# Kernel optimization log

Measured on AMD Instinct MI355X. Metric: run time of the kernel, lower is better.

## Reference

```python
import jax, jax.numpy as jnp
import numpy as np

N_EMBD = 768
N_HEAD = 12
HEAD_DIM = N_EMBD // N_HEAD
EPS = 1e-5


def _ln(x, g, b):
    mu = jnp.mean(x, axis=-1, keepdims=True)
    var = jnp.mean(jnp.square(x - mu), axis=-1, keepdims=True)
    return (x - mu) * jax.lax.rsqrt(var + EPS) * g + b


def _gelu(x):
    # GPT-2 / BERT tanh-approximate GELU (new_gelu)
    c = jnp.sqrt(2.0 / jnp.pi).astype(x.dtype)
    return 0.5 * x * (1.0 + jnp.tanh(c * (x + 0.044715 * x * x * x)))


def setup_inputs() -> dict:
    key = jax.random.key(0)
    ks = jax.random.split(key, 8)
    B, T, C = 4, 2048, N_EMBD
    s = 0.02
    return {
        "x": jax.random.normal(ks[0], (B, T, C), jnp.float32),
        "attention_mask": jnp.ones((B, T), jnp.float32),
        "ln1_g": jnp.ones((C,), jnp.float32),
        "ln1_b": jnp.zeros((C,), jnp.float32),
        "ln2_g": jnp.ones((C,), jnp.float32),
        "ln2_b": jnp.zeros((C,), jnp.float32),
        "W_attn": jax.random.normal(ks[1], (C, 3 * C), jnp.float32) * s,
        "b_attn": jnp.zeros((3 * C,), jnp.float32),
        "W_proj": jax.random.normal(ks[2], (C, C), jnp.float32) * s,
        "b_proj": jnp.zeros((C,), jnp.float32),
        "W_fc": jax.random.normal(ks[3], (C, 4 * C), jnp.float32) * s,
        "b_fc": jnp.zeros((4 * C,), jnp.float32),
        "W_out": jax.random.normal(ks[4], (4 * C, C), jnp.float32) * s,
        "b_out": jnp.zeros((C,), jnp.float32),
    }


def reference(x, attention_mask, ln1_g, ln1_b, ln2_g, ln2_b,
              W_attn, b_attn, W_proj, b_proj, W_fc, b_fc, W_out, b_out):
    B, T, C = x.shape
    H, D = N_HEAD, HEAD_DIM

    # --- attention sublayer ---
    h = _ln(x, ln1_g, ln1_b)
    qkv = h @ W_attn + b_attn                      # [B,T,3C]
    q, k, v = jnp.split(qkv, 3, axis=-1)
    q = q.reshape(B, T, H, D).transpose(0, 2, 1, 3)  # [B,H,T,D]
    k = k.reshape(B, T, H, D).transpose(0, 2, 1, 3)
    v = v.reshape(B, T, H, D).transpose(0, 2, 1, 3)

    att = jnp.einsum('bhqd,bhkd->bhqk', q, k) * (1.0 / jnp.sqrt(D).astype(x.dtype))
    mask_add = (1.0 - attention_mask)[:, None, None, :] * -10000.0  # [B,1,1,T]
    att = att + mask_add
    att = jax.nn.softmax(att, axis=-1)
    y = jnp.einsum('bhqk,bhkd->bhqd', att, v)      # [B,H,T,D]
    y = y.transpose(0, 2, 1, 3).reshape(B, T, C)
    x = x + (y @ W_proj + b_proj)

    # --- MLP sublayer ---
    h = _ln(x, ln2_g, ln2_b)
    h = _gelu(h @ W_fc + b_fc)
    x = x + (h @ W_out + b_out)
    return x
```

## Files before the change

### kernel.cpp

```cpp
#include <hip/hip_runtime.h>
#include <hip/hip_bf16.h>
#include <cstdint>

using short8   = __attribute__((ext_vector_type(8))) short;
using floatx4  = __attribute__((ext_vector_type(4))) float;
using ushort4v = __attribute__((ext_vector_type(4))) unsigned short;

#define DEVI static __device__ __forceinline__

DEVI unsigned short f2bf(float f) {
    union { float f; unsigned u; } v; v.f = f;
    unsigned r = v.u + 0x7FFFu + ((v.u >> 16) & 1u);
    return (unsigned short)(r >> 16);
}

DEVI unsigned cvtpk_bf16(float lo, float hi) {
    unsigned r;
    asm("v_cvt_pk_bf16_f32 %0, %1, %2" : "=v"(r) : "v"(lo), "v"(hi));
    return r;
}

typedef const __attribute__((address_space(1))) unsigned int gas_uint;
typedef __attribute__((address_space(3))) unsigned int las_uint;

DEVI void gload16(const void* g, void* l) {
    __builtin_amdgcn_global_load_lds((gas_uint*)g, (las_uint*)l, 16, 0, 0);
}

DEVI float gelu_f(float x) {
    float z = 0.7978845608028654f * (x + 0.044715f * x * x * x);
    float e = __expf(2.0f * z);
    float t = 1.0f - 2.0f / (e + 1.0f);
    return 0.5f * x * (1.0f + t);
}

#define QSCALE 0.18033688011112042f

__global__ __launch_bounds__(256)
void transpose_cast(const float* __restrict__ W, unsigned short* __restrict__ Wt,
                    int K, int N)
{
    __shared__ float tile[32][33];
    const int n0 = blockIdx.x * 32, k0 = blockIdx.y * 32;
    const int tx = threadIdx.x & 31, ty = threadIdx.x >> 5;
#pragma unroll
    for (int j = 0; j < 4; ++j)
        tile[ty + j * 8][tx] = W[(long)(k0 + ty + j * 8) * N + n0 + tx];
    __syncthreads();
#pragma unroll
    for (int j = 0; j < 4; ++j)
        Wt[(long)(n0 + ty + j * 8) * K + k0 + tx] = f2bf(tile[tx][ty + j * 8]);
}

__global__ __launch_bounds__(256)
void ln_cast_k(const float* __restrict__ x, const float* __restrict__ g,
               const float* __restrict__ beta, unsigned short* __restrict__ out)
{
    const int row = blockIdx.x;
    const int tid = threadIdx.x;
    const float* xr = x + (long)row * 768;
    float v0 = xr[tid], v1 = xr[tid + 256], v2 = xr[tid + 512];
    float s  = v0 + v1 + v2;
    float sq = v0 * v0 + v1 * v1 + v2 * v2;
#pragma unroll
    for (int m = 1; m < 64; m <<= 1) {
        s  += __shfl_xor(s, m);
        sq += __shfl_xor(sq, m);
    }
    __shared__ float ss[4], ssq[4];
    if ((tid & 63) == 0) { ss[tid >> 6] = s; ssq[tid >> 6] = sq; }
    __syncthreads();
    s  = ss[0] + ss[1] + ss[2] + ss[3];
    sq = ssq[0] + ssq[1] + ssq[2] + ssq[3];
    const float mean = s * (1.0f / 768.0f);
    const float var  = sq * (1.0f / 768.0f) - mean * mean;
    const float rstd = rsqrtf(var + 1e-5f);
    unsigned short* orow = out + (long)row * 768;
    orow[tid]       = f2bf((v0 - mean) * rstd * g[tid]       + beta[tid]);
    orow[tid + 256] = f2bf((v1 - mean) * rstd * g[tid + 256] + beta[tid + 256]);
    orow[tid + 512] = f2bf((v2 - mean) * rstd * g[tid + 512] + beta[tid + 512]);
}

template<int EPI>
__global__ __launch_bounds__(256)
void gemm128(const unsigned short* __restrict__ A,
             const unsigned short* __restrict__ Bt,
             const float* __restrict__ bias,
             const float* __restrict__ resid,
             unsigned short* __restrict__ ob0,
             unsigned short* __restrict__ ob1,
             unsigned short* __restrict__ ob2,
             float* __restrict__ of,
             int K, int N)
{
    const int mt = blockIdx.x, nt = blockIdx.y;
    const int tid = threadIdx.x;
    const int w = tid >> 6, lane = tid & 63;
    const int l16 = lane & 15, lq = lane >> 4;
    const int wm = w >> 1, wn = w & 1;

    __shared__ unsigned short As[128 * 64];
    __shared__ unsigned short Bs[128 * 64];

    const floatx4 fzero = {0.f, 0.f, 0.f, 0.f};
    floatx4 acc[4][4];
#pragma unroll
    for (int i = 0; i < 4; ++i)
#pragma unroll
        for (int j = 0; j < 4; ++j) acc[i][j] = fzero;

    const char* Abyte = (const char*)A + (long)mt * 128 * K * 2;
    const char* Bbyte = (const char*)Bt + (long)nt * 128 * K * 2;
    const int KT = K >> 6;

    for (int kt = 0; kt < KT; ++kt) {
        const int kbyte = kt * 128;
#pragma unroll
        for (int r4 = 0; r4 < 4; ++r4) {
            int base = (w * 4 + r4) * 1024;
            int loff = base + lane * 16;
            int row  = loff >> 7;
            int scb  = (loff & 127) ^ ((row & 7) << 4);
            gload16(Abyte + (long)row * (K * 2) + kbyte + scb, (char*)As + base);
            gload16(Bbyte + (long)row * (K * 2) + kbyte + scb, (char*)Bs + base);
        }
        __syncthreads();
#pragma unroll
        for (int ks = 0; ks < 2; ++ks) {
            const int kb = ks * 64 + lq * 16;
            short8 af[4], bfr[4];
#pragma unroll
            for (int f = 0; f < 4; ++f) {
                int ar = wm * 64 + f * 16 + l16;
                af[f]  = *(const short8*)((const char*)As + ar * 128 + (kb ^ ((ar & 7) << 4)));
                int br = wn * 64 + f * 16 + l16;
                bfr[f] = *(const short8*)((const char*)Bs + br * 128 + (kb ^ ((br & 7) << 4)));
            }
#pragma unroll
            for (int i = 0; i < 4; ++i)
#pragma unroll
                for (int j = 0; j < 4; ++j)
                    acc[i][j] = __builtin_amdgcn_mfma_f32_16x16x32_bf16(af[i], bfr[j], acc[i][j], 0, 0, 0);
        }
        __syncthreads();
    }

    const int col0 = nt * 128 + wn * 64;
    const int row0 = mt * 128 + wm * 64;
#pragma unroll
    for (int j = 0; j < 4; ++j) {
        const int col = col0 + j * 16 + l16;
        const float bv = bias[col];
#pragma unroll
        for (int i = 0; i < 4; ++i) {
            const int rowb = row0 + i * 16 + lq * 4;
            float v[4];
#pragma unroll
            for (int r = 0; r < 4; ++r) v[r] = acc[i][j][r] + bv;

            if (EPI == 0) {
                const int which = (col >= 1536) ? 2 : (col >= 768 ? 1 : 0);
                const int c = col - which * 768;
                const int hh = c >> 6, d = c & 63;
                const int bb = rowb >> 11;
                const int t  = rowb & 2047;
                if (which == 2) {
                    ushort4v pk;
#pragma unroll
                    for (int r = 0; r < 4; ++r) pk[r] = f2bf(v[r]);
                    const int tlo = t & 31;
                    const int tS  = (t & ~31) + ((tlo & 12) << 1) + ((tlo & 16) >> 2);
                    long vi = ((long)(bb * 12 + hh) * 64 + d) * 2048 + tS;
                    *(ushort4v*)(ob2 + vi) = pk;
                } else {
                    unsigned short* dst = (which == 0) ? ob0 : ob1;
                    const float qs = (which == 0) ? QSCALE : 1.0f;
                    long base = ((long)(bb * 12 + hh) * 2048 + t) * 64 + d;
#pragma unroll
                    for (int r = 0; r < 4; ++r) dst[base + (long)r * 64] = f2bf(v[r] * qs);
                }
            } else if (EPI == 1 || EPI == 3) {
#pragma unroll
                for (int r = 0; r < 4; ++r) {
                    long idx = (long)(rowb + r) * N + col;
                    of[idx] = v[r] + resid[idx];
                }
            } else {
#pragma unroll
                for (int r = 0; r < 4; ++r) {
                    long idx = (long)(rowb + r) * N + col;
                    ob0[idx] = f2bf(gelu_f(v[r]));
                }
            }
        }
    }
}

__global__ __launch_bounds__(256)
void attn_fwd(const unsigned short* __restrict__ q,
              const unsigned short* __restrict__ k,
              const unsigned short* __restrict__ vt,
              const float* __restrict__ mask,
              unsigned short* __restrict__ y)
{
    const int qt = blockIdx.x;
    const int bh = blockIdx.y;
    const int b = bh / 12, h = bh - b * 12;
    const int tid = threadIdx.x;
    const int w = tid >> 6, lane = tid & 63;
    const int l16 = lane & 15, lq = lane >> 4;

    __shared__ unsigned short Ks[128 * 64];
    __shared__ unsigned short Vs[64 * 128];
    __shared__ float madd[128];
    __shared__ int mq;

    if (tid == 0) mq = 0;
    __syncthreads();
    {
        const float* mrow = mask + (long)b * 2048 + tid * 8;
        int bad = 0;
#pragma unroll
        for (int j = 0; j < 8; ++j) bad |= (mrow[j] != 1.0f);
        if (bad) atomicOr(&mq, 1);
    }

    const unsigned short* qrow = q + ((long)bh * 2048 + qt * 64 + w * 16 + l16) * 64;
    const short8 qf0 = *(const short8*)(qrow + lq * 8);
    const short8 qf1 = *(const short8*)(qrow + 32 + lq * 8);

    const char* kg = (const char*)(k + (long)bh * 2048 * 64);
    const char* vg = (const char*)(vt + (long)bh * 64 * 2048);
    int koff[4], voff[4], lbase[4];
#pragma unroll
    for (int r4 = 0; r4 < 4; ++r4) {
        int base = (w * 4 + r4) * 1024;
        int loff = base + lane * 16;
        int rowK = loff >> 7;
        koff[r4] = rowK * 128 + ((loff & 127) ^ ((rowK & 7) << 4));
        int rowV = loff >> 8;
        voff[r4] = rowV * 4096 + ((loff & 255) ^ ((rowV & 7) << 4));
        lbase[r4] = base;
    }

    __syncthreads();
    const bool usemask = (mq != 0);

    const floatx4 fzero = {0.f, 0.f, 0.f, 0.f};
    floatx4 accO[4];
#pragma unroll
    for (int n = 0; n < 4; ++n) accO[n] = fzero;
    float m2 = -1e30f, lsum = 0.f;

    for (int kt = 0; kt < 16; ++kt) {
        const char* kgt = kg + (long)kt * 16384;
        const char* vgt = vg + kt * 256;
#pragma unroll
        for (int r4 = 0; r4 < 4; ++r4) {
            gload16(kgt + koff[r4], (char*)Ks + lbase[r4]);
            gload16(vgt + voff[r4], (char*)Vs + lbase[r4]);
        }
        if (usemask && tid < 128)
            madd[tid] = (1.0f - mask[b * 2048 + kt * 128 + tid]) * (-10000.0f * 1.4426950408889634f);
        __syncthreads();

        floatx4 st[8];
#pragma unroll
        for (int f = 0; f < 8; ++f) st[f] = fzero;
        __builtin_amdgcn_s_setprio(1);
#pragma unroll
        for (int f = 0; f < 8; ++f) {
            const int kr = f * 16 + l16;
            const int sw = (kr & 7) << 4;
            short8 ka0 = *(const short8*)((const char*)Ks + kr * 128 + ((lq * 16) ^ sw));
            short8 ka1 = *(const short8*)((const char*)Ks + kr * 128 + ((64 + lq * 16) ^ sw));
            st[f] = __builtin_amdgcn_mfma_f32_16x16x32_bf16(ka0, qf0, st[f], 0, 0, 0);
            st[f] = __builtin_amdgcn_mfma_f32_16x16x32_bf16(ka1, qf1, st[f], 0, 0, 0);
        }
        __builtin_amdgcn_s_setprio(0);

        if (usemask) {
#pragma unroll
            for (int f = 0; f < 8; ++f) {
                floatx4 md = *(const floatx4*)((const char*)madd + f * 64 + lq * 16);
                floatx4 t = st[f];
#pragma unroll
                for (int j = 0; j < 4; ++j) t[j] += md[j];
                st[f] = t;
            }
        }

        float rm = -3e38f;
#pragma unroll
        for (int f = 0; f < 8; ++f)
            rm = fmaxf(rm, fmaxf(fmaxf(st[f][0], st[f][1]), fmaxf(st[f][2], st[f][3])));
        rm = fmaxf(rm, __shfl_xor(rm, 16));
        rm = fmaxf(rm, __shfl_xor(rm, 32));

        if (!__all(rm <= m2 + 8.0f)) {
            const float mn = fmaxf(m2, rm);
            const float corr = exp2f(m2 - mn);
            m2 = mn;
            lsum *= corr;
            const float c0 = __shfl(corr, lq * 4 + 0);
            const float c1 = __shfl(corr, lq * 4 + 1);
            const float c2 = __shfl(corr, lq * 4 + 2);
            const float c3 = __shfl(corr, lq * 4 + 3);
#pragma unroll
            for (int n = 0; n < 4; ++n) {
                floatx4 t = accO[n];
                t[0] *= c0; t[1] *= c1; t[2] *= c2; t[3] *= c3;
                accO[n] = t;
            }
        }

        float rs = 0.f;
        unsigned pw[16];
#pragma unroll
        for (int f = 0; f < 8; ++f) {
            const floatx4 t = st[f];
            const float e0 = exp2f(t[0] - m2);
            const float e1 = exp2f(t[1] - m2);
            const float e2 = exp2f(t[2] - m2);
            const float e3 = exp2f(t[3] - m2);
            rs += (e0 + e1) + (e2 + e3);
            pw[f * 2]     = cvtpk_bf16(e0, e1);
            pw[f * 2 + 1] = cvtpk_bf16(e2, e3);
        }
        rs += __shfl_xor(rs, 16);
        rs += __shfl_xor(rs, 32);
        lsum += rs;

        __builtin_amdgcn_s_setprio(1);
#pragma unroll
        for (int c = 0; c < 4; ++c) {
            union { unsigned u[4]; short8 s8; } pu;
            pu.u[0] = pw[c * 4 + 0];
            pu.u[1] = pw[c * 4 + 1];
            pu.u[2] = pw[c * 4 + 2];
            pu.u[3] = pw[c * 4 + 3];
            const int kb2 = c * 64 + lq * 16;
#pragma unroll
            for (int n = 0; n < 4; ++n) {
                const int vr = n * 16 + l16;
                short8 vb = *(const short8*)((const char*)Vs + vr * 256 + (kb2 ^ ((vr & 7) << 4)));
                accO[n] = __builtin_amdgcn_mfma_f32_16x16x32_bf16(pu.s8, vb, accO[n], 0, 0, 0);
            }
        }
        __builtin_amdgcn_s_setprio(0);
        __syncthreads();
    }

    const float li = 1.0f / lsum;
    const float li0 = __shfl(li, lq * 4 + 0);
    const float li1 = __shfl(li, lq * 4 + 1);
    const float li2 = __shfl(li, lq * 4 + 2);
    const float li3 = __shfl(li, lq * 4 + 3);
    const float lir[4] = {li0, li1, li2, li3};
    unsigned short* ybase = y + ((long)(b * 2048 + qt * 64 + w * 16 + lq * 4)) * 768 + h * 64;
#pragma unroll
    for (int r = 0; r < 4; ++r) {
        unsigned short* yrow = ybase + (long)r * 768;
#pragma unroll
        for (int n = 0; n < 4; ++n)
            yrow[n * 16 + l16] = f2bf(accO[n][r] * lir[r]);
    }
}

extern "C" void kernel_launch(void* const* d_in, const int* in_sizes, int n_in,
                              void* d_out, int out_size, void* d_ws, size_t ws_size,
                              hipStream_t stream)
{
    const float* x     = (const float*)d_in[0];
    const float* amask = (const float*)d_in[1];
    const float* ln1g  = (const float*)d_in[2];
    const float* ln1b  = (const float*)d_in[3];
    const float* ln2g  = (const float*)d_in[4];
    const float* ln2b  = (const float*)d_in[5];
    const float* Wattn = (const float*)d_in[6];
    const float* battn = (const float*)d_in[7];
    const float* Wproj = (const float*)d_in[8];
    const float* bproj = (const float*)d_in[9];
    const float* Wfc   = (const float*)d_in[10];
    const float* bfc   = (const float*)d_in[11];
    const float* Wout  = (const float*)d_in[12];
    const float* bout  = (const float*)d_in[13];
    float* out = (float*)d_out;

    char* ws = (char*)d_ws;
    unsigned short* wt_attn = (unsigned short*)ws;  ws += (long)2304 * 768 * 2;
    unsigned short* wt_proj = (unsigned short*)ws;  ws += (long)768 * 768 * 2;
    unsigned short* wt_fc   = (unsigned short*)ws;  ws += (long)3072 * 768 * 2;
    unsigned short* wt_out  = (unsigned short*)ws;  ws += (long)768 * 3072 * 2;
    unsigned short* hbuf    = (unsigned short*)ws;  ws += (long)8192 * 768 * 2;
    unsigned short* qbuf    = (unsigned short*)ws;  ws += (long)48 * 2048 * 64 * 2;
    unsigned short* kbuf    = (unsigned short*)ws;  ws += (long)48 * 2048 * 64 * 2;
    unsigned short* vtbuf   = (unsigned short*)ws;  ws += (long)48 * 2048 * 64 * 2;
    unsigned short* ybuf    = (unsigned short*)ws;  ws += (long)8192 * 768 * 2;
    unsigned short* hfc     = (unsigned short*)ws;  ws += (long)8192 * 3072 * 2;

    transpose_cast<<<dim3(2304 / 32, 768 / 32), 256, 0, stream>>>(Wattn, wt_attn, 768, 2304);
    transpose_cast<<<dim3(768 / 32, 768 / 32), 256, 0, stream>>>(Wproj, wt_proj, 768, 768);
    transpose_cast<<<dim3(3072 / 32, 768 / 32), 256, 0, stream>>>(Wfc, wt_fc, 768, 3072);
    transpose_cast<<<dim3(768 / 32, 3072 / 32), 256, 0, stream>>>(Wout, wt_out, 3072, 768);

    ln_cast_k<<<8192, 256, 0, stream>>>(x, ln1g, ln1b, hbuf);

    gemm128<0><<<dim3(64, 18), 256, 0, stream>>>(hbuf, wt_attn, battn, nullptr,
                                                 qbuf, kbuf, vtbuf, nullptr, 768, 2304);

    attn_fwd<<<dim3(32, 48), 256, 0, stream>>>(qbuf, kbuf, vtbuf, amask, ybuf);

    gemm128<1><<<dim3(64, 6), 256, 0, stream>>>(ybuf, wt_proj, bproj, x,
                                                nullptr, nullptr, nullptr, out, 768, 768);

    ln_cast_k<<<8192, 256, 0, stream>>>(out, ln2g, ln2b, hbuf);

    gemm128<2><<<dim3(64, 24), 256, 0, stream>>>(hbuf, wt_fc, bfc, nullptr,
                                                 hfc, nullptr, nullptr, nullptr, 768, 3072);

    gemm128<3><<<dim3(64, 6), 256, 0, stream>>>(hfc, wt_out, bout, out,
                                                nullptr, nullptr, nullptr, out, 3072, 768);
}
```

Before: 341.3 us.

## Double-buffer K/V tiles in attention and shrink key tile to 64

The attention kernel now keeps two LDS buffers for the K, V and mask tiles. It prefetches the next 64-key tile while the current one is being computed, and needs only one barrier per iteration instead of the old load-then-compute pattern. The key tile size drops from 128 to 64 so the two buffers fit in the same LDS footprint. The aim is to hide global-to-LDS latency behind the MFMA work. The cost is twice as many loop iterations, which means more online-softmax rescale and reduction overhead per key.

Result: no change. 344.2 us (+0.8%).

```diff
diff --git a/kernel.cpp b/kernel.cpp
--- a/kernel.cpp
+++ b/kernel.cpp
@@ -210,9 +210,9 @@
     const int w = tid >> 6, lane = tid & 63;
     const int l16 = lane & 15, lq = lane >> 4;
 
-    __shared__ unsigned short Ks[128 * 64];
-    __shared__ unsigned short Vs[64 * 128];
-    __shared__ float madd[128];
+    __shared__ unsigned short Ks[2][64 * 64];
+    __shared__ unsigned short Vs[2][64 * 64];
+    __shared__ float madd[2][64];
     __shared__ int mq;
 
     if (tid == 0) mq = 0;
@@ -231,49 +231,62 @@
 
     const char* kg = (const char*)(k + (long)bh * 2048 * 64);
     const char* vg = (const char*)(vt + (long)bh * 64 * 2048);
-    int koff[4], voff[4], lbase[4];
-#pragma unroll
-    for (int r4 = 0; r4 < 4; ++r4) {
-        int base = (w * 4 + r4) * 1024;
-        int loff = base + lane * 16;
-        int rowK = loff >> 7;
-        koff[r4] = rowK * 128 + ((loff & 127) ^ ((rowK & 7) << 4));
-        int rowV = loff >> 8;
-        voff[r4] = rowV * 4096 + ((loff & 255) ^ ((rowV & 7) << 4));
-        lbase[r4] = base;
+    int koff[2], voff[2], lb[2];
+#pragma unroll
+    for (int r2 = 0; r2 < 2; ++r2) {
+        int loff = r2 * 4096 + tid * 16;
+        int row  = loff >> 7;
+        int scb  = (loff & 127) ^ ((row & 7) << 4);
+        koff[r2] = row * 128 + scb;
+        voff[r2] = row * 4096 + scb;
+        lb[r2]   = loff;
     }
 
     __syncthreads();
     const bool usemask = (mq != 0);
 
+#pragma unroll
+    for (int r2 = 0; r2 < 2; ++r2) {
+        gload16(kg + koff[r2], (char*)Ks[0] + lb[r2]);
+        gload16(vg + voff[r2], (char*)Vs[0] + lb[r2]);
+    }
+    if (usemask && tid < 64)
+        madd[0][tid] = (1.0f - mask[b * 2048 + tid]) * (-10000.0f * 1.4426950408889634f);
+    __syncthreads();
+
     const floatx4 fzero = {0.f, 0.f, 0.f, 0.f};
     floatx4 accO[4];
 #pragma unroll
     for (int n = 0; n < 4; ++n) accO[n] = fzero;
     float m2 = -1e30f, lsum = 0.f;
 
-    for (int kt = 0; kt < 16; ++kt) {
-        const char* kgt = kg + (long)kt * 16384;
-        const char* vgt = vg + kt * 256;
-#pragma unroll
-        for (int r4 = 0; r4 < 4; ++r4) {
-            gload16(kgt + koff[r4], (char*)Ks + lbase[r4]);
-            gload16(vgt + voff[r4], (char*)Vs + lbase[r4]);
-        }
-        if (usemask && tid < 128)
-            madd[tid] = (1.0f - mask[b * 2048 + kt * 128 + tid]) * (-10000.0f * 1.4426950408889634f);
-        __syncthreads();
-
-        floatx4 st[8];
-#pragma unroll
-        for (int f = 0; f < 8; ++f) st[f] = fzero;
+    for (int kt = 0; kt < 32; ++kt) {
+        const int cur = kt & 1;
+
+        if (kt < 31) {
+            const char* kgt = kg + (long)(kt + 1) * 8192;
+            const char* vgt = vg + (kt + 1) * 128;
+#pragma unroll
+            for (int r2 = 0; r2 < 2; ++r2) {
+                gload16(kgt + koff[r2], (char*)Ks[cur ^ 1] + lb[r2]);
+                gload16(vgt + voff[r2], (char*)Vs[cur ^ 1] + lb[r2]);
+            }
+            if (usemask && tid < 64)
+                madd[cur ^ 1][tid] = (1.0f - mask[b * 2048 + (kt + 1) * 64 + tid]) * (-10000.0f * 1.4426950408889634f);
+        }
+
+        const char* Kc = (const char*)Ks[cur];
+        const char* Vc = (const char*)Vs[cur];
+        floatx4 st[4];
+#pragma unroll
+        for (int f = 0; f < 4; ++f) st[f] = fzero;
         __builtin_amdgcn_s_setprio(1);
 #pragma unroll
-        for (int f = 0; f < 8; ++f) {
+        for (int f = 0; f < 4; ++f) {
             const int kr = f * 16 + l16;
             const int sw = (kr & 7) << 4;
-            short8 ka0 = *(const short8*)((const char*)Ks + kr * 128 + ((lq * 16) ^ sw));
-            short8 ka1 = *(const short8*)((const char*)Ks + kr * 128 + ((64 + lq * 16) ^ sw));
+            short8 ka0 = *(const short8*)(Kc + kr * 128 + ((lq * 16) ^ sw));
+            short8 ka1 = *(const short8*)(Kc + kr * 128 + ((64 + lq * 16) ^ sw));
             st[f] = __builtin_amdgcn_mfma_f32_16x16x32_bf16(ka0, qf0, st[f], 0, 0, 0);
             st[f] = __builtin_amdgcn_mfma_f32_16x16x32_bf16(ka1, qf1, st[f], 0, 0, 0);
         }
@@ -281,8 +294,8 @@
 
         if (usemask) {
 #pragma unroll
-            for (int f = 0; f < 8; ++f) {
-                floatx4 md = *(const floatx4*)((const char*)madd + f * 64 + lq * 16);
+            for (int f = 0; f < 4; ++f) {
+                floatx4 md = *(const floatx4*)((const char*)madd[cur] + f * 64 + lq * 16);
                 floatx4 t = st[f];
 #pragma unroll
                 for (int j = 0; j < 4; ++j) t[j] += md[j];
@@ -292,7 +305,7 @@
 
         float rm = -3e38f;
 #pragma unroll
-        for (int f = 0; f < 8; ++f)
+        for (int f = 0; f < 4; ++f)
             rm = fmaxf(rm, fmaxf(fmaxf(st[f][0], st[f][1]), fmaxf(st[f][2], st[f][3])));
         rm = fmaxf(rm, __shfl_xor(rm, 16));
         rm = fmaxf(rm, __shfl_xor(rm, 32));
@@ -315,9 +328,9 @@
         }
 
         float rs = 0.f;
-        unsigned pw[16];
-#pragma unroll
-        for (int f = 0; f < 8; ++f) {
+        unsigned pw[8];
+#pragma unroll
+        for (int f = 0; f < 4; ++f) {
             const floatx4 t = st[f];
             const float e0 = exp2f(t[0] - m2);
             const float e1 = exp2f(t[1] - m2);
@@ -333,7 +346,7 @@
 
         __builtin_amdgcn_s_setprio(1);
 #pragma unroll
-        for (int c = 0; c < 4; ++c) {
+        for (int c = 0; c < 2; ++c) {
             union { unsigned u[4]; short8 s8; } pu;
             pu.u[0] = pw[c * 4 + 0];
             pu.u[1] = pw[c * 4 + 1];
@@ -343,11 +356,12 @@
 #pragma unroll
             for (int n = 0; n < 4; ++n) {
                 const int vr = n * 16 + l16;
-                short8 vb = *(const short8*)((const char*)Vs + vr * 256 + (kb2 ^ ((vr & 7) << 4)));
+                short8 vb = *(const short8*)(Vc + vr * 128 + (kb2 ^ ((vr & 7) << 4)));
                 accO[n] = __builtin_amdgcn_mfma_f32_16x16x32_bf16(pu.s8, vb, accO[n], 0, 0, 0);
             }
         }
         __builtin_amdgcn_s_setprio(0);
+
         __syncthreads();
     }
 
```

## Add 256x256-tile double-buffered GEMM for QKV and FC projections

Applied to the files above, without the earlier changes.

Introduces a 512-thread GEMM kernel with 256x256 output tiles, XOR-swizzled LDS, double-buffered direct global-to-LDS loads interleaved with MFMA quads, and setprio around MFMA bursts. It is used for the QKV and FC projections, while the narrow-N projections stay on the 128-tile kernel, which now handles only the residual epilogue. The larger tiles raise data reuse per block and overlap loads with compute. The cost is 128KB of LDS per block and far fewer blocks (288 and 384), which may underfill the GPU's CUs.

After: 346.6 us. Within noise of the previous version (+1.5%).

```diff
diff --git a/kernel.cpp b/kernel.cpp
--- a/kernel.cpp
+++ b/kernel.cpp
@@ -25,6 +25,12 @@
 
 DEVI void gload16(const void* g, void* l) {
     __builtin_amdgcn_global_load_lds((gas_uint*)g, (las_uint*)l, 16, 0, 0);
+}
+
+DEVI void barrier_raw() {
+    asm volatile("" ::: "memory");
+    __builtin_amdgcn_s_barrier();
+    asm volatile("" ::: "memory");
 }
 
 DEVI float gelu_f(float x) {
@@ -81,15 +87,38 @@
     orow[tid + 512] = f2bf((v2 - mean) * rstd * g[tid + 512] + beta[tid + 512]);
 }
 
+DEVI void epi_qkv(int col, int rowb, const float* bias,
+                  unsigned short* ob0, unsigned short* ob1, unsigned short* ob2,
+                  const float* v)
+{
+    const int which = (col >= 1536) ? 2 : (col >= 768 ? 1 : 0);
+    const int c = col - which * 768;
+    const int hh = c >> 6, d = c & 63;
+    const int bb = rowb >> 11;
+    const int t  = rowb & 2047;
+    if (which == 2) {
+        ushort4v pk;
+#pragma unroll
+        for (int r = 0; r < 4; ++r) pk[r] = f2bf(v[r]);
+        const int tlo = t & 31;
+        const int tS  = (t & ~31) + ((tlo & 12) << 1) + ((tlo & 16) >> 2);
+        long vi = ((long)(bb * 12 + hh) * 64 + d) * 2048 + tS;
+        *(ushort4v*)(ob2 + vi) = pk;
+    } else {
+        unsigned short* dst = (which == 0) ? ob0 : ob1;
+        const float qs = (which == 0) ? QSCALE : 1.0f;
+        long base = ((long)(bb * 12 + hh) * 2048 + t) * 64 + d;
+#pragma unroll
+        for (int r = 0; r < 4; ++r) dst[base + (long)r * 64] = f2bf(v[r] * qs);
+    }
+}
+
 template<int EPI>
 __global__ __launch_bounds__(256)
 void gemm128(const unsigned short* __restrict__ A,
              const unsigned short* __restrict__ Bt,
              const float* __restrict__ bias,
              const float* __restrict__ resid,
-             unsigned short* __restrict__ ob0,
-             unsigned short* __restrict__ ob1,
-             unsigned short* __restrict__ ob2,
              float* __restrict__ of,
              int K, int N)
 {
@@ -154,37 +183,166 @@
 #pragma unroll
         for (int i = 0; i < 4; ++i) {
             const int rowb = row0 + i * 16 + lq * 4;
+#pragma unroll
+            for (int r = 0; r < 4; ++r) {
+                long idx = (long)(rowb + r) * N + col;
+                of[idx] = acc[i][j][r] + bv + resid[idx];
+            }
+        }
+    }
+}
+
+DEVI short8 lds_frag(const char* base, int row, int kb) {
+    return *(const short8*)(base + row * 128 + (kb ^ ((row & 7) << 4)));
+}
+
+template<int MFO, int NFO>
+DEVI void mfma_quad(floatx4 (&acc)[8][4], const short8 (&a)[4][2], const short8 (&b)[4][2]) {
+    __builtin_amdgcn_s_setprio(1);
+#pragma unroll
+    for (int mm = 0; mm < 4; ++mm)
+#pragma unroll
+        for (int nn = 0; nn < 2; ++nn)
+#pragma unroll
+            for (int ks = 0; ks < 2; ++ks)
+                acc[MFO + mm][NFO + nn] =
+                    __builtin_amdgcn_mfma_f32_16x16x32_bf16(a[mm][ks], b[NFO + nn][ks],
+                                                            acc[MFO + mm][NFO + nn], 0, 0, 0);
+    __builtin_amdgcn_s_setprio(0);
+}
+
+template<int EPI>
+__global__ __launch_bounds__(512, 2)
+void gemm256(const unsigned short* __restrict__ A,
+             const unsigned short* __restrict__ Bt,
+             const float* __restrict__ bias,
+             unsigned short* __restrict__ ob0,
+             unsigned short* __restrict__ ob1,
+             unsigned short* __restrict__ ob2,
+             int K, int N)
+{
+    extern __shared__ char smem[];
+    char* As0 = smem;
+    char* As1 = smem + 32768;
+    char* Bs0 = smem + 65536;
+    char* Bs1 = smem + 98304;
+
+    const int mt = blockIdx.x, nt = blockIdx.y;
+    const int tid = threadIdx.x;
+    const int w = tid >> 6, lane = tid & 63;
+    const int l16 = lane & 15, lq = lane >> 4;
+    const int wm = w >> 2, wn = w & 3;
+
+    const int K2 = K * 2;
+    const char* Ab = (const char*)A + (long)mt * 256 * K2;
+    const char* Bb = (const char*)Bt + (long)nt * 256 * K2;
+
+    int loff_[4], soff_[4];
+#pragma unroll
+    for (int i = 0; i < 4; ++i) {
+        const int lo = i * 8192 + tid * 16;
+        const int srow = lo >> 7;
+        loff_[i] = lo;
+        soff_[i] = srow * K2 + ((lo & 127) ^ ((srow & 7) << 4));
+    }
+
+    const floatx4 fzero = {0.f, 0.f, 0.f, 0.f};
+    floatx4 acc[8][4];
+#pragma unroll
+    for (int i = 0; i < 8; ++i)
+#pragma unroll
+        for (int j = 0; j < 4; ++j) acc[i][j] = fzero;
+
+    const int KT = K >> 6;
+
+#pragma unroll
+    for (int i = 0; i < 4; ++i) {
+        gload16(Ab + soff_[i], As0 + loff_[i]);
+        gload16(Bb + soff_[i], Bs0 + loff_[i]);
+    }
+#pragma unroll
+    for (int i = 0; i < 4; ++i) {
+        gload16(Ab + soff_[i] + 128, As1 + loff_[i]);
+        gload16(Bb + soff_[i] + 128, Bs1 + loff_[i]);
+    }
+    asm volatile("s_waitcnt vmcnt(8)" ::: "memory");
+    barrier_raw();
+
+    short8 a[4][2], b[4][2];
+
+    for (int kt = 0; kt < KT; ++kt) {
+        const bool odd = (kt & 1) != 0;
+        const char* Ac = odd ? As1 : As0;
+        const char* Bc = odd ? Bs1 : Bs0;
+        char* Asg = odd ? As1 : As0;
+        char* Bsg = odd ? Bs1 : Bs0;
+        const bool dost = (kt + 2 < KT);
+        const int kst = (kt + 2) * 128;
+
+#pragma unroll
+        for (int mm = 0; mm < 4; ++mm)
+#pragma unroll
+            for (int ks = 0; ks < 2; ++ks)
+                a[mm][ks] = lds_frag(Ac, wm * 128 + mm * 16 + l16, ks * 64 + lq * 16);
+#pragma unroll
+        for (int nn = 0; nn < 2; ++nn)
+#pragma unroll
+            for (int ks = 0; ks < 2; ++ks)
+                b[nn][ks] = lds_frag(Bc, wn * 64 + nn * 16 + l16, ks * 64 + lq * 16);
+        barrier_raw();
+        mfma_quad<0, 0>(acc, a, b);
+        barrier_raw();
+
+#pragma unroll
+        for (int nn = 2; nn < 4; ++nn)
+#pragma unroll
+            for (int ks = 0; ks < 2; ++ks)
+                b[nn][ks] = lds_frag(Bc, wn * 64 + nn * 16 + l16, ks * 64 + lq * 16);
+        barrier_raw();
+        mfma_quad<0, 2>(acc, a, b);
+        barrier_raw();
+
+#pragma unroll
+        for (int mm = 0; mm < 4; ++mm)
+#pragma unroll
+            for (int ks = 0; ks < 2; ++ks)
+                a[mm][ks] = lds_frag(Ac, wm * 128 + 64 + mm * 16 + l16, ks * 64 + lq * 16);
+        if (dost) {
+#pragma unroll
+            for (int i = 0; i < 4; ++i)
+                gload16(Bb + soff_[i] + kst, Bsg + loff_[i]);
+        }
+        barrier_raw();
+        mfma_quad<4, 2>(acc, a, b);
+        barrier_raw();
+
+        if (dost) {
+#pragma unroll
+            for (int i = 0; i < 4; ++i)
+                gload16(Ab + soff_[i] + kst, Asg + loff_[i]);
+        }
+        barrier_raw();
+        mfma_quad<4, 0>(acc, a, b);
+
+        if (dost) asm volatile("s_waitcnt vmcnt(8)" ::: "memory");
+        else      asm volatile("s_waitcnt vmcnt(0)" ::: "memory");
+        barrier_raw();
+    }
+
+    const int row0 = mt * 256 + wm * 128;
+    const int col0 = nt * 256 + wn * 64;
+#pragma unroll
+    for (int nf = 0; nf < 4; ++nf) {
+        const int col = col0 + nf * 16 + l16;
+        const float bv = bias[col];
+#pragma unroll
+        for (int mf = 0; mf < 8; ++mf) {
+            const int rowb = row0 + mf * 16 + lq * 4;
             float v[4];
 #pragma unroll
-            for (int r = 0; r < 4; ++r) v[r] = acc[i][j][r] + bv;
-
+            for (int r = 0; r < 4; ++r) v[r] = acc[mf][nf][r] + bv;
             if (EPI == 0) {
-                const int which = (col >= 1536) ? 2 : (col >= 768 ? 1 : 0);
-                const int c = col - which * 768;
-                const int hh = c >> 6, d = c & 63;
-                const int bb = rowb >> 11;
-                const int t  = rowb & 2047;
-                if (which == 2) {
-                    ushort4v pk;
-#pragma unroll
-                    for (int r = 0; r < 4; ++r) pk[r] = f2bf(v[r]);
-                    const int tlo = t & 31;
-                    const int tS  = (t & ~31) + ((tlo & 12) << 1) + ((tlo & 16) >> 2);
-                    long vi = ((long)(bb * 12 + hh) * 64 + d) * 2048 + tS;
-                    *(ushort4v*)(ob2 + vi) = pk;
-                } else {
-                    unsigned short* dst = (which == 0) ? ob0 : ob1;
-                    const float qs = (which == 0) ? QSCALE : 1.0f;
-                    long base = ((long)(bb * 12 + hh) * 2048 + t) * 64 + d;
-#pragma unroll
-                    for (int r = 0; r < 4; ++r) dst[base + (long)r * 64] = f2bf(v[r] * qs);
-                }
-            } else if (EPI == 1 || EPI == 3) {
-#pragma unroll
-                for (int r = 0; r < 4; ++r) {
-                    long idx = (long)(rowb + r) * N + col;
-                    of[idx] = v[r] + resid[idx];
-                }
+                epi_qkv(col, rowb, bias, ob0, ob1, ob2, v);
             } else {
 #pragma unroll
                 for (int r = 0; r < 4; ++r) {
@@ -399,6 +557,11 @@
     unsigned short* ybuf    = (unsigned short*)ws;  ws += (long)8192 * 768 * 2;
     unsigned short* hfc     = (unsigned short*)ws;  ws += (long)8192 * 3072 * 2;
 
+    (void)hipFuncSetAttribute((const void*)gemm256<0>,
+                              hipFuncAttributeMaxDynamicSharedMemorySize, 131072);
+    (void)hipFuncSetAttribute((const void*)gemm256<2>,
+                              hipFuncAttributeMaxDynamicSharedMemorySize, 131072);
+
     transpose_cast<<<dim3(2304 / 32, 768 / 32), 256, 0, stream>>>(Wattn, wt_attn, 768, 2304);
     transpose_cast<<<dim3(768 / 32, 768 / 32), 256, 0, stream>>>(Wproj, wt_proj, 768, 768);
     transpose_cast<<<dim3(3072 / 32, 768 / 32), 256, 0, stream>>>(Wfc, wt_fc, 768, 3072);
@@ -406,19 +569,17 @@
 
     ln_cast_k<<<8192, 256, 0, stream>>>(x, ln1g, ln1b, hbuf);
 
-    gemm128<0><<<dim3(64, 18), 256, 0, stream>>>(hbuf, wt_attn, battn, nullptr,
-                                                 qbuf, kbuf, vtbuf, nullptr, 768, 2304);
+    gemm256<0><<<dim3(32, 9), 512, 131072, stream>>>(hbuf, wt_attn, battn,
+                                                     qbuf, kbuf, vtbuf, 768, 2304);
 
     attn_fwd<<<dim3(32, 48), 256, 0, stream>>>(qbuf, kbuf, vtbuf, amask, ybuf);
 
-    gemm128<1><<<dim3(64, 6), 256, 0, stream>>>(ybuf, wt_proj, bproj, x,
-                                                nullptr, nullptr, nullptr, out, 768, 768);
+    gemm128<1><<<dim3(64, 6), 256, 0, stream>>>(ybuf, wt_proj, bproj, x, out, 768, 768);
 
     ln_cast_k<<<8192, 256, 0, stream>>>(out, ln2g, ln2b, hbuf);
 
-    gemm128<2><<<dim3(64, 24), 256, 0, stream>>>(hbuf, wt_fc, bfc, nullptr,
-                                                 hfc, nullptr, nullptr, nullptr, 768, 3072);
-
-    gemm128<3><<<dim3(64, 6), 256, 0, stream>>>(hfc, wt_out, bout, out,
-                                                nullptr, nullptr, nullptr, out, 3072, 768);
-}
+    gemm256<2><<<dim3(32, 12), 512, 131072, stream>>>(hbuf, wt_fc, bfc,
+                                                      hfc, nullptr, nullptr, 768, 3072);
+
+    gemm128<3><<<dim3(64, 6), 256, 0, stream>>>(hfc, wt_out, bout, out, out, 3072, 768);
+}
```
